# Kernel optimization log

Hardware: AMD Instinct MI355X
Metric: run time of the kernel (lower is better)

The kernel has to match this reference:

```python
import jax, jax.numpy as jnp
import numpy as np

N_BINS = 32
EPS = 6.4 / 256.0
LO = -3.2 - EPS / 2.0
HI = 3.2 - EPS / 2.0
BIN_W = (HI - LO) / N_BINS


def _rgb_uv_hist_one(img):
    # img: [3, H, W] -> [3, 32, 32] sqrt-normalized RGB-uv histogram
    C, H, W = img.shape
    # cv2 INTER_NEAREST downsample: src index = floor(dst * scale)
    ry = jnp.floor(jnp.arange(N_BINS) * (H / N_BINS)).astype(jnp.int32)
    rx = jnp.floor(jnp.arange(N_BINS) * (W / N_BINS)).astype(jnp.int32)
    small = img[:, ry][:, :, rx]                 # [3, 32, 32]
    px = small.reshape(3, -1)                    # [3, 1024]
    valid = jnp.all(px > 0, axis=0)              # pixels with all channels > 0
    Iy = jnp.sqrt(jnp.sum(px * px, axis=0))      # per-pixel L2 norm (weights)
    w = jnp.where(valid, Iy, 0.0)
    px_safe = jnp.where(px > 0, px, 1.0)         # guard log for masked pixels
    logs = jnp.log(px_safe)                      # [3, 1024]
    hists = []
    for i in range(3):
        r = [j for j in range(3) if j != i]
        Iu = logs[i] - logs[r[1]]
        Iv = logs[i] - logs[r[0]]
        inb = valid & (Iu >= LO) & (Iu <= HI) & (Iv >= LO) & (Iv <= HI)
        iu = jnp.clip(jnp.floor((Iu - LO) / BIN_W).astype(jnp.int32), 0, N_BINS - 1)
        iv = jnp.clip(jnp.floor((Iv - LO) / BIN_W).astype(jnp.int32), 0, N_BINS - 1)
        flat = iu * N_BINS + iv                  # histogram2d: rows=Iu, cols=Iv
        h = jnp.zeros(N_BINS * N_BINS, dtype=px.dtype).at[flat].add(jnp.where(inb, w, 0.0))
        h = h / jnp.sum(h)
        hists.append(jnp.sqrt(h).reshape(N_BINS, N_BINS))
    return jnp.stack(hists)                      # [3, 32, 32]


def setup_inputs() -> dict:
    key = jax.random.key(0)
    ks = jax.random.split(key, 7)
    B, H, W = 32, 512, 512
    inp_img = jax.random.uniform(ks[0], (B, 3, H, W), dtype=jnp.float32)
    s = 0.02
    return {
        "inp_img": inp_img,
        "W1": jax.random.normal(ks[1], (1024, 3072), jnp.float32) * s,
        "b1": jax.random.normal(ks[2], (1024,), jnp.float32) * s,
        "W2": jax.random.normal(ks[3], (512, 1024), jnp.float32) * s,
        "b2": jax.random.normal(ks[4], (512,), jnp.float32) * s,
        "W3": jax.random.normal(ks[5], (256, 512), jnp.float32) * s,
        "b3": jax.random.normal(ks[6], (256,), jnp.float32) * s,
    }


def reference(inp_img, W1, b1, W2, b2, W3, b3):
    B = inp_img.shape[0]
    hist = jax.vmap(_rgb_uv_hist_one)(inp_img).reshape(B, -1)  # [B, 3072]
    hist = jax.lax.stop_gradient(hist)  # original code detaches the histogram
    x = jax.nn.relu(hist @ W1.T + b1)
    x = jax.nn.relu(x @ W2.T + b2)
    x = jax.nn.relu(x @ W3.T + b3)      # [B, 256]
    return x[..., None, None]            # [B, 256, 1, 1]
```

## Files before the change

kernel.cpp:

```cpp
#include <hip/hip_runtime.h>
#include <math.h>

#define IMG_H 512
#define IMG_W 512
#define HWSZ (IMG_H * IMG_W)
#define BATCH 32

__device__ __forceinline__ size_t xidx(int k, int b) {
    return (size_t)(k >> 1) * 64 + b * 2 + (k & 1);
}

__global__ __launch_bounds__(1024) void hist_bias_k(const float* __restrict__ img,
                                                    float* __restrict__ histT,
                                                    const float* __restrict__ b1,
                                                    const float* __restrict__ b2,
                                                    float* __restrict__ y1,
                                                    float* __restrict__ y2)
{
    if (blockIdx.x >= 32) {
        const int t = (blockIdx.x - 32) * 1024 + threadIdx.x;
        {
            const int o = ((t >> 6) << 1) | (t & 1);
            y1[t] = b1[o];
        }
        if (t < 16384) {
            const int o = ((t >> 6) << 1) | (t & 1);
            y2[t] = b2[o];
        }
        return;
    }

    const int b   = blockIdx.x;
    const int tid = threadIdx.x;

    __shared__ float hh[3][1024];
    __shared__ float red[17];

    hh[0][tid] = 0.f;
    hh[1][tid] = 0.f;
    hh[2][tid] = 0.f;
    __syncthreads();

    const int py  = tid >> 5;
    const int pxi = tid & 31;
    const size_t base = (size_t)b * 3 * HWSZ + (size_t)(py * 16) * IMG_W + (size_t)(pxi * 16);

    const float r  = img[base];
    const float g  = img[base + HWSZ];
    const float bl = img[base + 2 * HWSZ];

    const bool valid = (r > 0.f) && (g > 0.f) && (bl > 0.f);

    const float LOc = (float)(-3.2 - (6.4 / 256.0) * 0.5);
    const float HIc = (float)( 3.2 - (6.4 / 256.0) * 0.5);
    const float BWc = (float)(((3.2 - (6.4 / 256.0) * 0.5) - (-3.2 - (6.4 / 256.0) * 0.5)) / 32.0);

    if (valid) {
        const float w  = sqrtf(r * r + g * g + bl * bl);
        const float lr = logf(r);
        const float lg = logf(g);
        const float lb = logf(bl);

        float us[3] = { lr - lb, lg - lb, lb - lg };
        float vs[3] = { lr - lg, lg - lr, lb - lr };

        #pragma unroll
        for (int i = 0; i < 3; ++i) {
            const float U = us[i];
            const float V = vs[i];
            if (U >= LOc && U <= HIc && V >= LOc && V <= HIc) {
                int iu = (int)floorf((U - LOc) / BWc); iu = iu < 31 ? iu : 31;
                int iv = (int)floorf((V - LOc) / BWc); iv = iv < 31 ? iv : 31;
                atomicAdd(&hh[i][iu * 32 + iv], w);
            }
        }
    }
    __syncthreads();

    #pragma unroll
    for (int i = 0; i < 3; ++i) {
        float v = hh[i][tid];
        float t = v;
        #pragma unroll
        for (int off = 32; off; off >>= 1) t += __shfl_down(t, off);
        if ((tid & 63) == 0) red[tid >> 6] = t;
        __syncthreads();
        if (tid == 0) {
            float s = 0.f;
            #pragma unroll
            for (int j = 0; j < 16; ++j) s += red[j];
            red[16] = 1.0f / s;
        }
        __syncthreads();
        const float inv = red[16];
        histT[xidx(i * 1024 + tid, b)] = sqrtf(v * inv);
        __syncthreads();
    }
}

template <int K, int N, int S, bool RELU>
__global__ __launch_bounds__(256) void gemm_atomic_k(const float* __restrict__ xT,
                                                     const float* __restrict__ W,
                                                     float* __restrict__ y)
{
    constexpr int C  = K / S;
    constexpr int NG = N / 8;

    const int wave = (blockIdx.x * 256 + threadIdx.x) >> 6;
    const int lane = threadIdx.x & 63;
    const int b    = lane & 31;
    const int o0   = __builtin_amdgcn_readfirstlane((wave % NG) * 8);
    const int k0   = __builtin_amdgcn_readfirstlane((wave / NG) * C);

    const float* Wr[8];
    #pragma unroll
    for (int j = 0; j < 8; ++j) Wr[j] = W + (size_t)(o0 + j) * K + k0;

    const float2* xp = reinterpret_cast<const float2*>(xT + (size_t)k0 * BATCH) + b;

    float acc[8] = {0.f, 0.f, 0.f, 0.f, 0.f, 0.f, 0.f, 0.f};

    #pragma unroll 4
    for (int kk2 = 0; kk2 < C / 2; ++kk2) {
        float2 v = xp[kk2 * BATCH];
        if (RELU) { v.x = fmaxf(v.x, 0.f); v.y = fmaxf(v.y, 0.f); }
        #pragma unroll
        for (int j = 0; j < 8; ++j) {
            acc[j] = fmaf(v.x, Wr[j][2 * kk2],     acc[j]);
            acc[j] = fmaf(v.y, Wr[j][2 * kk2 + 1], acc[j]);
        }
    }

    if (lane < 32) {
        #pragma unroll
        for (int j = 0; j < 8; ++j)
            atomicAdd(&y[xidx(o0 + j, b)], acc[j]);
    }
}

template <int K, int N>
__global__ __launch_bounds__(256) void linear_out_k(const float* __restrict__ xT,
                                                    const float* __restrict__ W,
                                                    const float* __restrict__ bias,
                                                    float* __restrict__ out)
{
    constexpr int C = K / 4;
    const int og   = blockIdx.x;
    const int w    = threadIdx.x >> 6;
    const int lane = threadIdx.x & 63;
    const int b    = lane & 31;
    const int o0   = og * 8;
    const int k0   = __builtin_amdgcn_readfirstlane(w * C);

    const float* Wr[8];
    #pragma unroll
    for (int j = 0; j < 8; ++j) Wr[j] = W + (size_t)(o0 + j) * K + k0;

    const float2* xp = reinterpret_cast<const float2*>(xT + (size_t)k0 * BATCH) + b;

    float acc[8] = {0.f, 0.f, 0.f, 0.f, 0.f, 0.f, 0.f, 0.f};

    #pragma unroll 4
    for (int kk2 = 0; kk2 < C / 2; ++kk2) {
        float2 v = xp[kk2 * BATCH];
        v.x = fmaxf(v.x, 0.f); v.y = fmaxf(v.y, 0.f);
        #pragma unroll
        for (int j = 0; j < 8; ++j) {
            acc[j] = fmaf(v.x, Wr[j][2 * kk2],     acc[j]);
            acc[j] = fmaf(v.y, Wr[j][2 * kk2 + 1], acc[j]);
        }
    }

    __shared__ float part[4][8][32];
    if (lane < 32) {
        #pragma unroll
        for (int j = 0; j < 8; ++j) part[w][j][b] = acc[j];
    }
    __syncthreads();

    const int j  = threadIdx.x >> 5;
    const int b2 = threadIdx.x & 31;
    float s = part[0][j][b2] + part[1][j][b2] + part[2][j][b2] + part[3][j][b2]
            + bias[o0 + j];
    out[b2 * N + o0 + j] = fmaxf(s, 0.f);
}

extern "C" void kernel_launch(void* const* d_in, const int* in_sizes, int n_in,
                              void* d_out, int out_size, void* d_ws, size_t ws_size,
                              hipStream_t stream)
{
    const float* img = (const float*)d_in[0];
    const float* W1  = (const float*)d_in[1];
    const float* b1  = (const float*)d_in[2];
    const float* W2  = (const float*)d_in[3];
    const float* b2  = (const float*)d_in[4];
    const float* W3  = (const float*)d_in[5];
    const float* b3  = (const float*)d_in[6];
    float* out = (float*)d_out;

    float* ws = (float*)d_ws;
    float* histT = ws;
    float* y1    = histT + 3072 * BATCH;
    float* y2    = y1    + 1024 * BATCH;

    hist_bias_k<<<64, 1024, 0, stream>>>(img, histT, b1, b2, y1, y2);

    gemm_atomic_k<3072, 1024, 16, false><<<512, 256, 0, stream>>>(histT, W1, y1);
    gemm_atomic_k<1024,  512, 16, true ><<<256, 256, 0, stream>>>(y1, W2, y2);
    linear_out_k<512, 256><<<32, 256, 0, stream>>>(y2, W3, b3, out);
}
```

Measured before the change: 194.7 us.

## Split histogram into per-quarter partial blocks plus separate normalize kernel

The histogram kernel now spreads each image over four 256-thread blocks, 128 histogram blocks instead of 32, each writing a partial 3x1024 histogram to workspace. A new kernel sums the four partials per image, normalizes and writes the transposed layout. The bias initialization moves to extra 256-thread blocks. This raises parallelism in the gather-bound stage, but adds a kernel launch and about 1.5MB of partial-histogram traffic.

```diff
diff --git a/kernel.cpp b/kernel.cpp
--- a/kernel.cpp
+++ b/kernel.cpp
@@ -10,40 +10,38 @@
     return (size_t)(k >> 1) * 64 + b * 2 + (k & 1);
 }
 
-__global__ __launch_bounds__(1024) void hist_bias_k(const float* __restrict__ img,
-                                                    float* __restrict__ histT,
-                                                    const float* __restrict__ b1,
-                                                    const float* __restrict__ b2,
-                                                    float* __restrict__ y1,
-                                                    float* __restrict__ y2)
-{
-    if (blockIdx.x >= 32) {
-        const int t = (blockIdx.x - 32) * 1024 + threadIdx.x;
-        {
+__global__ __launch_bounds__(256) void hist_part_k(const float* __restrict__ img,
+                                                   float* __restrict__ hp,
+                                                   const float* __restrict__ b1,
+                                                   const float* __restrict__ b2,
+                                                   float* __restrict__ y1,
+                                                   float* __restrict__ y2)
+{
+    if (blockIdx.x >= 128) {
+        const int t = (blockIdx.x - 128) * 256 + threadIdx.x;
+        if (t < 32768) {
             const int o = ((t >> 6) << 1) | (t & 1);
             y1[t] = b1[o];
-        }
-        if (t < 16384) {
-            const int o = ((t >> 6) << 1) | (t & 1);
-            y2[t] = b2[o];
+        } else {
+            const int u = t - 32768;
+            const int o = ((u >> 6) << 1) | (u & 1);
+            y2[u] = b2[o];
         }
         return;
     }
 
-    const int b   = blockIdx.x;
-    const int tid = threadIdx.x;
-
-    __shared__ float hh[3][1024];
-    __shared__ float red[17];
-
-    hh[0][tid] = 0.f;
-    hh[1][tid] = 0.f;
-    hh[2][tid] = 0.f;
-    __syncthreads();
-
-    const int py  = tid >> 5;
-    const int pxi = tid & 31;
-    const size_t base = (size_t)b * 3 * HWSZ + (size_t)(py * 16) * IMG_W + (size_t)(pxi * 16);
+    const int img_i = blockIdx.x >> 2;
+    const int blk   = blockIdx.x & 3;
+    const int tid   = threadIdx.x;
+
+    __shared__ float hh[3072];
+    for (int i = tid; i < 3072; i += 256) hh[i] = 0.f;
+    __syncthreads();
+
+    const int p  = blk * 256 + tid;
+    const int py = p >> 5;
+    const int px = p & 31;
+    const size_t base = (size_t)img_i * 3 * HWSZ + (size_t)(py * 16) * IMG_W + (size_t)(px * 16);
 
     const float r  = img[base];
     const float g  = img[base + HWSZ];
@@ -71,31 +69,55 @@
             if (U >= LOc && U <= HIc && V >= LOc && V <= HIc) {
                 int iu = (int)floorf((U - LOc) / BWc); iu = iu < 31 ? iu : 31;
                 int iv = (int)floorf((V - LOc) / BWc); iv = iv < 31 ? iv : 31;
-                atomicAdd(&hh[i][iu * 32 + iv], w);
+                atomicAdd(&hh[i * 1024 + iu * 32 + iv], w);
             }
         }
     }
     __syncthreads();
 
-    #pragma unroll
-    for (int i = 0; i < 3; ++i) {
-        float v = hh[i][tid];
-        float t = v;
-        #pragma unroll
-        for (int off = 32; off; off >>= 1) t += __shfl_down(t, off);
-        if ((tid & 63) == 0) red[tid >> 6] = t;
-        __syncthreads();
-        if (tid == 0) {
-            float s = 0.f;
-            #pragma unroll
-            for (int j = 0; j < 16; ++j) s += red[j];
-            red[16] = 1.0f / s;
-        }
-        __syncthreads();
-        const float inv = red[16];
-        histT[xidx(i * 1024 + tid, b)] = sqrtf(v * inv);
-        __syncthreads();
-    }
+    float* outp = hp + (size_t)blockIdx.x * 3072;
+    for (int i = tid; i < 3072; i += 256) outp[i] = hh[i];
+}
+
+__global__ __launch_bounds__(1024) void hist_norm_k(const float* __restrict__ hp,
+                                                    float* __restrict__ histT)
+{
+    const int img_i = blockIdx.x;
+    const int tid   = threadIdx.x;
+    const int wid   = tid >> 6;
+    const int lane  = tid & 63;
+
+    __shared__ float red[3][16];
+    __shared__ float invs[3];
+    const float* base = hp + (size_t)img_i * 4 * 3072;
+
+    float v[3];
+    #pragma unroll
+    for (int c = 0; c < 3; ++c) {
+        const int idx = c * 1024 + tid;
+        v[c] = base[idx] + base[3072 + idx] + base[2 * 3072 + idx] + base[3 * 3072 + idx];
+    }
+
+    float t0 = v[0], t1 = v[1], t2 = v[2];
+    #pragma unroll
+    for (int off = 32; off; off >>= 1) {
+        t0 += __shfl_down(t0, off);
+        t1 += __shfl_down(t1, off);
+        t2 += __shfl_down(t2, off);
+    }
+    if (lane == 0) { red[0][wid] = t0; red[1][wid] = t1; red[2][wid] = t2; }
+    __syncthreads();
+    if (tid < 3) {
+        float s = 0.f;
+        #pragma unroll
+        for (int j = 0; j < 16; ++j) s += red[tid][j];
+        invs[tid] = 1.0f / s;
+    }
+    __syncthreads();
+
+    #pragma unroll
+    for (int c = 0; c < 3; ++c)
+        histT[xidx(c * 1024 + tid, img_i)] = sqrtf(v[c] * invs[c]);
 }
 
 template <int K, int N, int S, bool RELU>
@@ -199,11 +221,13 @@
     float* out = (float*)d_out;
 
     float* ws = (float*)d_ws;
-    float* histT = ws;
+    float* hp    = ws;
+    float* histT = hp    + 128 * 3072;
     float* y1    = histT + 3072 * BATCH;
     float* y2    = y1    + 1024 * BATCH;
 
-    hist_bias_k<<<64, 1024, 0, stream>>>(img, histT, b1, b2, y1, y2);
+    hist_part_k<<<320, 256, 0, stream>>>(img, hp, b1, b2, y1, y2);
+    hist_norm_k<<<BATCH, 1024, 0, stream>>>(hp, histT);
 
     gemm_atomic_k<3072, 1024, 16, false><<<512, 256, 0, stream>>>(histT, W1, y1);
     gemm_atomic_k<1024,  512, 16, true ><<<256, 256, 0, stream>>>(y1, W2, y2);
```

Result: no change. 191.9 us (-1.5%).
